# Optimization experiments

Hardware: AMD Instinct MI355X
Metric: run time of the kernel (lower is better)

The kernel has to match this reference:

```python
import jax, jax.numpy as jnp
import numpy as np
from jax import lax

B, N = 16, 4096
S1, S2, K = 512, 256, 32
EPS = 1e-5


def setup_inputs() -> dict:
    key = jax.random.key(0)
    ks = jax.random.split(key, 8)
    p = lambda k, shape: jax.random.normal(k, shape, jnp.float32) * 0.05
    return {
        "x": jax.random.normal(ks[0], (B, 3, N), jnp.float32),
        "w1": p(ks[1], (64, 3)),
        "w2": p(ks[2], (64, 64)),
        "g1": jnp.ones(64, jnp.float32), "b1": jnp.zeros(64, jnp.float32),
        "g2": jnp.ones(64, jnp.float32), "b2": jnp.zeros(64, jnp.float32),
        "sg1_w1": p(ks[3], (128, 128)), "sg1_w2": p(ks[4], (128, 128)),
        "sg1_g1": jnp.ones(128, jnp.float32), "sg1_b1": jnp.zeros(128, jnp.float32),
        "sg1_g2": jnp.ones(128, jnp.float32), "sg1_b2": jnp.zeros(128, jnp.float32),
        "sg2_w1": p(ks[5], (256, 256)), "sg2_w2": p(ks[6], (256, 256)),
        "sg2_g1": jnp.ones(256, jnp.float32), "sg2_b1": jnp.zeros(256, jnp.float32),
        "sg2_g2": jnp.ones(256, jnp.float32), "sg2_b2": jnp.zeros(256, jnp.float32),
    }


def fps(coords, s):
    # furthest point sampling, starts at index 0 (as pointnet2 CUDA kernel)
    Bc, Nc, _ = coords.shape
    def step(carry, _):
        dist, far = carry
        centroid = jnp.take_along_axis(coords, far[:, None, None], axis=1)  # [B,1,3]
        d = jnp.sum((coords - centroid) ** 2, -1)                            # [B,N]
        dist = jnp.minimum(dist, d)
        return (dist, jnp.argmax(dist, -1)), far
    init = (jnp.full((Bc, Nc), 1e10, coords.dtype), jnp.zeros((Bc,), jnp.int32))
    _, idxs = lax.scan(step, init, None, length=s)
    return idxs.T  # [B,s]


def gather(pts, idx):
    # pts [B,N,C], idx [B,...] -> [B,...,C]
    return jax.vmap(lambda p, i: p[i])(pts, idx)


def sqdist(a, b):
    # [B,S,3],[B,N,3] -> [B,S,N]
    return (jnp.sum(a ** 2, -1)[..., None] + jnp.sum(b ** 2, -1)[:, None, :]
            - 2.0 * jnp.einsum('bsc,bnc->bsn', a, b))


def bn_relu_grouped(y, g, b):
    # y [B,s,k,O]; BatchNorm1d over (B*s, O, k) => stats over (0,1,2)
    m = y.mean((0, 1, 2), keepdims=True)
    v = y.var((0, 1, 2), keepdims=True)
    return jax.nn.relu((y - m) / jnp.sqrt(v + EPS) * g + b)


def sg_block(f_bnc, coords, s, w1, g1, b1, w2, g2, b2):
    # f_bnc [B,N,C]; coords [B,N,3]
    fidx = fps(coords, s)                      # [B,s]
    new_xyz = gather(coords, fidx)             # [B,s,3]
    new_feat = gather(f_bnc, fidx)             # [B,s,C]
    d = sqdist(new_xyz, coords)                # [B,s,N]
    _, knn_idx = lax.top_k(-d, K)              # [B,s,K]
    grouped = gather(f_bnc, knn_idx)           # [B,s,K,C]
    center = new_feat[:, :, None]              # [B,s,1,C]
    agg = jnp.concatenate([grouped - center,
                           jnp.broadcast_to(center, grouped.shape)], -1)  # [B,s,K,2C]
    y = bn_relu_grouped(jnp.einsum('bskd,od->bsko', agg, w1), g1, b1)
    y = bn_relu_grouped(jnp.einsum('bskd,od->bsko', y, w2), g2, b2)
    return new_xyz, y.max(2)                   # [B,s,O]


def point_cbr(f, w, g, b):
    # f [B,C,N]; conv1d k=1 + BN (stats over (0,2)) + relu
    y = jnp.einsum('bcn,oc->bon', f, w)
    m = y.mean((0, 2), keepdims=True)
    v = y.var((0, 2), keepdims=True)
    return jax.nn.relu((y - m) / jnp.sqrt(v + EPS) * g[None, :, None] + b[None, :, None])


def reference(x, w1, w2, g1, b1, g2, b2,
              sg1_w1, sg1_w2, sg1_g1, sg1_b1, sg1_g2, sg1_b2,
              sg2_w1, sg2_w2, sg2_g1, sg2_b1, sg2_g2, sg2_b2):
    xyz = x.transpose(0, 2, 1)                                  # [B,N,3]
    f = point_cbr(point_cbr(x, w1, g1, b1), w2, g2, b2)         # [B,64,N]
    xyz1, f1 = sg_block(f.transpose(0, 2, 1), xyz, S1,
                        sg1_w1, sg1_g1, sg1_b1, sg1_w2, sg1_g2, sg1_b2)  # f1 [B,S1,128]
    _, f2 = sg_block(f1, xyz1, S2,
                     sg2_w1, sg2_g1, sg2_b1, sg2_w2, sg2_g2, sg2_b2)     # [B,S2,256]
    return f2.transpose(0, 2, 1)                                # [B,256,S2]
```

## Files before the change

### kernel.cpp

```cpp
#include <hip/hip_runtime.h>

#define EPSF 1e-5f
#define NBINS 64
#define STATS_REGION 32768

using short8  = __attribute__((ext_vector_type(8))) short;
using float4v = __attribute__((ext_vector_type(4))) float;

__device__ __forceinline__ unsigned short f2bf(float f){
    unsigned u = __float_as_uint(f);
    unsigned r = u + 0x7FFFu + ((u >> 16) & 1u);
    return (unsigned short)(r >> 16);
}
__device__ __forceinline__ float bf2f(unsigned short h){
    return __uint_as_float(((unsigned)h) << 16);
}
__device__ __forceinline__ unsigned monou(float f){
    unsigned u = __float_as_uint(f);
    return u ^ (((unsigned)((int)u >> 31)) | 0x80000000u);
}

template<int CTRL, int RMASK>
__device__ __forceinline__ float fmax_dpp(float x){
    int xi = __float_as_int(x);
    int yi = __builtin_amdgcn_update_dpp(xi, xi, CTRL, RMASK, 0xf, false);
    return fmaxf(x, __int_as_float(yi));
}
__device__ __forceinline__ float wave_max_dpp(float x){
    x = fmax_dpp<0x111, 0xf>(x);
    x = fmax_dpp<0x112, 0xf>(x);
    x = fmax_dpp<0x114, 0xf>(x);
    x = fmax_dpp<0x118, 0xf>(x);
    x = fmax_dpp<0x142, 0xa>(x);
    x = fmax_dpp<0x143, 0xc>(x);
    return __int_as_float(__builtin_amdgcn_readlane(__float_as_int(x), 63));
}


__global__ __launch_bounds__(256) void pc1_kernel(const float* __restrict__ x,
                                                  const float* __restrict__ w1,
                                                  float* __restrict__ y){
    __shared__ float w[192];
    int t = threadIdx.x;
    if (t < 192) w[t] = w1[t];
    __syncthreads();
    int gid = blockIdx.x * 256 + t;
    int b = gid >> 12;
    int n = gid & 4095;
    const float* xb = x + (size_t)b * 3 * 4096;
    float x0 = xb[n], x1 = xb[4096 + n], x2 = xb[8192 + n];
    float* yb = y + (size_t)b * 64 * 4096;
    #pragma unroll
    for (int o = 0; o < 64; o++){
        float v = x0 * w[o*3] + x1 * w[o*3+1] + x2 * w[o*3+2];
        yb[(size_t)o * 4096 + n] = v;
    }
}

template<int C, int NN>
__global__ __launch_bounds__(256) void stats_bcn_kernel(const float* __restrict__ y,
                                                        float* __restrict__ sums){
    int blk = blockIdx.x;
    int c = blk % C;
    const float* p = y + (size_t)blk * NN;
    float s = 0.f, q = 0.f;
    for (int i = threadIdx.x; i < NN; i += 256){ float v = p[i]; s += v; q += v*v; }
    for (int o = 32; o > 0; o >>= 1){ s += __shfl_down(s, o, 64); q += __shfl_down(q, o, 64); }
    __shared__ float ls[4], lq[4];
    int w = threadIdx.x >> 6;
    if ((threadIdx.x & 63) == 0){ ls[w] = s; lq[w] = q; }
    __syncthreads();
    if (threadIdx.x == 0){
        s = ls[0] + ls[1] + ls[2] + ls[3];
        q = lq[0] + lq[1] + lq[2] + lq[3];
        atomicAdd(&sums[c], s);
        atomicAdd(&sums[C + c], q);
    }
}

__global__ void bn_finalize_kernel(const float* __restrict__ sums,
                                   const float* __restrict__ g,
                                   const float* __restrict__ bb,
                                   float* __restrict__ ss, int C, int NB, float invCnt){
    int c = blockIdx.x * blockDim.x + threadIdx.x;
    if (c < C){
        float s = 0.f, q = 0.f;
        for (int bin = 0; bin < NB; bin++){
            s += sums[bin * 2 * C + c];
            q += sums[bin * 2 * C + C + c];
        }
        float m = s * invCnt;
        float v = q * invCnt - m * m;
        float sc = g[c] / sqrtf(v + EPSF);
        ss[c] = sc;
        ss[C + c] = bb[c] - m * sc;
    }
}

__global__ __launch_bounds__(256) void pc2_kernel(const float* __restrict__ y1,
                                                  const float* __restrict__ w2,
                                                  const float* __restrict__ ss,
                                                  float* __restrict__ y2){
    __shared__ float wt[64*64];
    __shared__ float lss[128];
    int t = threadIdx.x;
    for (int i = t; i < 4096; i += 256){ int o = i & 63, c = i >> 6; wt[c*64+o] = w2[o*64+c]; }
    if (t < 128) lss[t] = ss[t];
    __syncthreads();
    int gid = blockIdx.x * 256 + t;
    int b = gid >> 12, n = gid & 4095;
    const float* yb = y1 + (size_t)b * 64 * 4096;
    float acc[64];
    #pragma unroll
    for (int o = 0; o < 64; o++) acc[o] = 0.f;
    for (int c = 0; c < 64; c++){
        float v = yb[(size_t)c * 4096 + n];
        v = fmaxf(v * lss[c] + lss[64 + c], 0.f);
        #pragma unroll
        for (int o = 0; o < 64; o++) acc[o] += v * wt[c*64 + o];
    }
    float* ob = y2 + (size_t)b * 64 * 4096;
    #pragma unroll
    for (int o = 0; o < 64; o++) ob[(size_t)o * 4096 + n] = acc[o];
}

__global__ __launch_bounds__(256) void transpose_f_kernel(const float* __restrict__ y2,
                                                          const float* __restrict__ ss,
                                                          float* __restrict__ f){
    __shared__ float tile[64][65];
    __shared__ float lss[128];
    int t = threadIdx.x;
    if (t < 128) lss[t] = ss[t];
    __syncthreads();
    int blk = blockIdx.x;
    int b = blk >> 6;
    int nb = (blk & 63) * 64;
    const float* yb = y2 + (size_t)b * 64 * 4096;
    #pragma unroll
    for (int r = 0; r < 16; r++){
        int c = r * 4 + (t >> 6);
        int n = t & 63;
        float v = yb[(size_t)c * 4096 + nb + n];
        tile[c][n] = fmaxf(v * lss[c] + lss[64 + c], 0.f);
    }
    __syncthreads();
    float* fb = f + (size_t)b * 4096 * 64;
    #pragma unroll
    for (int r = 0; r < 16; r++){
        int n = r * 4 + (t >> 6);
        int c = t & 63;
        fb[(size_t)(nb + n) * 64 + c] = tile[c][n];
    }
}

template<int NP, int SO, int TPB, bool STRIDED>
__global__ __launch_bounds__(TPB) void fps_kernel(const float* __restrict__ coords,
                                                  int* __restrict__ fidx,
                                                  float* __restrict__ xyz_out){
    __shared__ float lx[NP], ly[NP], lz[NP];
    constexpr int W = TPB / 64;
    __shared__ unsigned long long red[2][W];
    const int b = blockIdx.x, t = threadIdx.x;
    constexpr int P = NP / TPB;
    const float* cb = coords + (size_t)b * 3 * NP;
    float px[P], py[P], pz[P], dist[P];
    #pragma unroll
    for (int i = 0; i < P; i++){
        int n = i * TPB + t;
        float X, Y, Z;
        if (STRIDED){ X = cb[n]; Y = cb[NP + n]; Z = cb[2*NP + n]; }
        else        { X = cb[n*3]; Y = cb[n*3+1]; Z = cb[n*3+2]; }
        lx[n] = X; ly[n] = Y; lz[n] = Z;
    }
    __syncthreads();
    #pragma unroll
    for (int i = 0; i < P; i++){
        int n = t * P + i;
        px[i] = lx[n]; py[i] = ly[n]; pz[i] = lz[n];
        dist[i] = 1e10f;
    }
    int cur = 0;
    for (int it = 0; it < SO; ++it){
        if (t == 0){
            fidx[b * SO + it] = cur;
            float* xo = xyz_out + ((size_t)b * SO + it) * 3;
            xo[0] = lx[cur]; xo[1] = ly[cur]; xo[2] = lz[cur];
        }
        float cx = lx[cur], cy = ly[cur], cz = lz[cur];
        float bd = -1.f;
        int bn = 0;
        {
            #pragma clang fp contract(off)
            #pragma unroll
            for (int i = 0; i < P; i++){
                float dx = px[i] - cx, dy = py[i] - cy, dz = pz[i] - cz;
                float d = (dx*dx + dy*dy) + dz*dz;
                float nd = fminf(dist[i], d);
                dist[i] = nd;
                if (nd > bd){ bd = nd; bn = t * P + i; }
            }
        }
        float wm = wave_max_dpp(bd);
        unsigned long long msk = __ballot(bd == wm);
        int wl = (int)(__ffsll(msk) - 1);
        int n_w = __builtin_amdgcn_readlane(bn, wl);
        if constexpr (W == 1){
            cur = n_w;
        } else {
            int par = it & 1;
            if ((t & 63) == 0){
                red[par][t >> 6] = ((unsigned long long)__float_as_uint(wm) << 32)
                                 | (unsigned)(0xFFFFFFFFu - (unsigned)n_w);
            }
            __syncthreads();
            unsigned long long best = red[par][0];
            #pragma unroll
            for (int j = 1; j < W; j++){
                unsigned long long v = red[par][j];
                best = best > v ? best : v;
            }
            cur = (int)(0xFFFFFFFFu - (unsigned)(best & 0xFFFFFFFFull));
        }
    }
}


template<int NC, int SO, bool STRIDED>
__global__ __launch_bounds__(64) void knn_kernel(const float* __restrict__ coords,
                                                 const float* __restrict__ samp,
                                                 int* __restrict__ knno){
    const int blk = blockIdx.x;
    const int b = blk / SO, s = blk % SO;
    const int lane = threadIdx.x;
    const float* cb = coords + (size_t)b * 3 * NC;
    const float* a = samp + ((size_t)b * SO + s) * 3;
    float ax = a[0], ay = a[1], az = a[2];
    float asq = ax*ax + ay*ay + az*az;
    constexpr int J = NC / 64;
    unsigned long long t8[8];
    #pragma unroll
    for (int i = 0; i < 8; i++) t8[i] = ~0ULL;
    for (int j = 0; j < J; j++){
        int n = j * 64 + lane;
        float bx, by, bz;
        if (STRIDED){ bx = cb[n]; by = cb[NC + n]; bz = cb[2*NC + n]; }
        else        { bx = cb[n*3]; by = cb[n*3+1]; bz = cb[n*3+2]; }
        float bsq = bx*bx + by*by + bz*bz;
        float dot = ax*bx + ay*by + az*bz;
        float d = (asq + bsq) - 2.0f * dot;
        unsigned long long key = ((unsigned long long)monou(d) << 32) | (unsigned)n;
        if (key < t8[7]){
            t8[7] = key;
            #pragma unroll
            for (int i = 6; i >= 0; i--){
                if (t8[i] > t8[i+1]){ unsigned long long tm = t8[i]; t8[i] = t8[i+1]; t8[i+1] = tm; }
            }
        }
    }
    unsigned long long cur = t8[0];
    int myout = 0;
    bool bad = false;
    int popped = 0;
    for (int r = 0; r < 32; r++){
        unsigned long long m = cur;
        #pragma unroll
        for (int o2 = 32; o2 > 0; o2 >>= 1){
            unsigned long long v = __shfl_xor(m, o2, 64);
            m = m < v ? m : v;
        }
        if (lane == r) myout = (int)(unsigned)(m & 0xFFFFFFFFull);
        if (cur == m){
            #pragma unroll
            for (int i = 0; i < 7; i++) t8[i] = t8[i+1];
            t8[7] = ~0ULL;
            cur = t8[0];
            popped++;
            if (J > 8 && popped == 8 && r < 31) bad = true;
        }
    }
    if (__any(bad)){
        unsigned long long last = 0;
        for (int r = 0; r < 32; r++){
            unsigned long long mk = ~0ULL;
            for (int j = 0; j < J; j++){
                int n = j * 64 + lane;
                float bx, by, bz;
                if (STRIDED){ bx = cb[n]; by = cb[NC + n]; bz = cb[2*NC + n]; }
                else        { bx = cb[n*3]; by = cb[n*3+1]; bz = cb[n*3+2]; }
                float bsq = bx*bx + by*by + bz*bz;
                float dot = ax*bx + ay*by + az*bz;
                float d = (asq + bsq) - 2.0f * dot;
                unsigned long long key = ((unsigned long long)monou(d) << 32) | (unsigned)n;
                if (key > last && key < mk) mk = key;
            }
            unsigned long long m = mk;
            #pragma unroll
            for (int o2 = 32; o2 > 0; o2 >>= 1){
                unsigned long long v = __shfl_xor(m, o2, 64);
                m = m < v ? m : v;
            }
            if (lane == r) myout = (int)(unsigned)(m & 0xFFFFFFFFull);
            last = m;
        }
    }
    if (lane < 32) knno[((size_t)b * SO + s) * 32 + lane] = myout;
}


template<int O, int D>
__global__ __launch_bounds__(256) void pack_w_kernel(const float* __restrict__ w,
                                                     unsigned short* __restrict__ pk){
    int tid = blockIdx.x * 256 + threadIdx.x;
    constexpr int CH = D / 32;
    constexpr int TOT = (O/16) * CH * 64;
    if (tid >= TOT) return;
    int lane = tid & 63;
    int fc = tid >> 6;
    int ch = fc % CH;
    int ot = fc / CH;
    int o  = ot * 16 + (lane & 15);
    int kb = ch * 32 + (lane >> 4) * 8;
    #pragma unroll
    for (int j = 0; j < 8; j++) pk[(size_t)tid * 8 + j] = f2bf(w[(size_t)o * D + kb + j]);
}

template<int D, int O>
__device__ __forceinline__ void mfma_compute_store(const short* A, const short* wp,
                                                   unsigned short* Y, float* lsum, float* lsq,
                                                   int blk, int t){
    constexpr int RS = D + 8;
    constexpr int CH = D / 32;
    constexpr int OT = O / 16;
    constexpr int OPW = OT / 4;
    int lane = t & 63, wv = t >> 6;
    int col = lane & 15, quad = lane >> 4;
    for (int oi = 0; oi < OPW; ++oi){
        int ot = wv * OPW + oi;
        for (int mt = 0; mt < 4; ++mt){
            float4v acc = {0.f, 0.f, 0.f, 0.f};
            #pragma unroll
            for (int ch = 0; ch < CH; ++ch){
                short8 a  = *(const short8*)(A + (mt*16 + col) * RS + ch*32 + quad*8);
                short8 bf = *(const short8*)(wp + ((size_t)(ot*CH + ch) * 64 + lane) * 8);
                acc = __builtin_amdgcn_mfma_f32_16x16x32_bf16(a, bf, acc, 0, 0, 0);
            }
            float s4 = 0.f, q4 = 0.f;
            size_t rowbase = (size_t)blk * 64 + mt * 16 + quad * 4;
            #pragma unroll
            for (int r = 0; r < 4; r++){
                float v = acc[r];
                s4 += v; q4 += v * v;
                Y[(rowbase + r) * O + ot * 16 + col] = f2bf(v);
            }
            s4 += __shfl_xor(s4, 16, 64); s4 += __shfl_xor(s4, 32, 64);
            q4 += __shfl_xor(q4, 16, 64); q4 += __shfl_xor(q4, 32, 64);
            if (quad == 0){ lsum[ot*16 + col] += s4; lsq[ot*16 + col] += q4; }
        }
    }
}

template<int DH, int O, int S, int NPTS>
__global__ __launch_bounds__(256) void gemm1_kernel(const float* __restrict__ fsrc,
                                                    const int* __restrict__ fidx,
                                                    const int* __restrict__ knn,
                                                    const short* __restrict__ wp,
                                                    unsigned short* __restrict__ Y,
                                                    float* __restrict__ sums){
    constexpr int D = 2 * DH;
    constexpr int RS = D + 8;
    __shared__ __align__(16) short A[64 * RS];
    __shared__ float lsum[O], lsq[O];
    int t = threadIdx.x;
    for (int i = t; i < O; i += 256){ lsum[i] = 0.f; lsq[i] = 0.f; }
    int blk = blockIdx.x;
    for (int g = 0; g < 2; ++g){
        int gid = blk * 2 + g;
        int b = gid / S;
        int cidx = fidx[gid];
        const float* fc = fsrc + ((size_t)b * NPTS + cidx) * DH;
        int kk = t >> 3;
        int p  = t & 7;
        int nb = knn[(size_t)gid * 32 + kk];
        const float* fn = fsrc + ((size_t)b * NPTS + nb) * DH;
        constexpr int E = D / 8;
        int d0 = p * E;
        short* row = A + (g * 32 + kk) * RS;
        #pragma unroll
        for (int e = 0; e < E; e++){
            int d = d0 + e;
            float v = (d < DH) ? (fn[d] - fc[d]) : fc[d - DH];
            row[d] = (short)f2bf(v);
        }
    }
    __syncthreads();
    mfma_compute_store<D, O>(A, wp, Y, lsum, lsq, blk, t);
    __syncthreads();
    float* dst = sums + (size_t)(blk & (NBINS - 1)) * 2 * O;
    for (int i = t; i < O; i += 256){
        atomicAdd(&dst[i], lsum[i]);
        atomicAdd(&dst[O + i], lsq[i]);
    }
}

template<int D, int O>
__global__ __launch_bounds__(256) void gemm2_kernel(const unsigned short* __restrict__ Yin,
                                                    const float* __restrict__ ss,
                                                    const short* __restrict__ wp,
                                                    unsigned short* __restrict__ Y,
                                                    float* __restrict__ sums){
    constexpr int RS = D + 8;
    __shared__ __align__(16) short A[64 * RS];
    __shared__ float lsum[O], lsq[O];
    __shared__ float lss[2 * D];
    int t = threadIdx.x;
    for (int i = t; i < O; i += 256){ lsum[i] = 0.f; lsq[i] = 0.f; }
    for (int i = t; i < 2*D; i += 256) lss[i] = ss[i];
    __syncthreads();
    int blk = blockIdx.x;
    {
        int row = t >> 2;
        int d0 = (t & 3) * (D / 4);
        const unsigned short* src = Yin + ((size_t)blk * 64 + row) * D + d0;
        short* dst = A + row * RS + d0;
        #pragma unroll
        for (int e = 0; e < D/4; e++){
            float v = bf2f(src[e]);
            int d = d0 + e;
            v = fmaxf(v * lss[d] + lss[D + d], 0.f);
            dst[e] = (short)f2bf(v);
        }
    }
    __syncthreads();
    mfma_compute_store<D, O>(A, wp, Y, lsum, lsq, blk, t);
    __syncthreads();
    float* dst = sums + (size_t)(blk & (NBINS - 1)) * 2 * O;
    for (int i = t; i < O; i += 256){
        atomicAdd(&dst[i], lsum[i]);
        atomicAdd(&dst[O + i], lsq[i]);
    }
}

template<int O>
__global__ __launch_bounds__(256) void maxk_kernel(const unsigned short* __restrict__ Y,
                                                   const float* __restrict__ ss,
                                                   float* __restrict__ out){
    int gid = blockIdx.x * 256 + threadIdx.x;
    int o = gid % O;
    int r = gid / O;
    float sc = ss[o], sh = ss[O + o];
    const unsigned short* p = Y + (size_t)r * 32 * O + o;
    float m = -1e30f;
    #pragma unroll 8
    for (int k = 0; k < 32; k++){
        float v = bf2f(p[(size_t)k * O]);
        m = fmaxf(m, v * sc + sh);
    }
    out[gid] = fmaxf(m, 0.f);
}

__global__ __launch_bounds__(256) void transpose_out_kernel(const float* __restrict__ in,
                                                            float* __restrict__ out){
    __shared__ float tile[64][65];
    int blk = blockIdx.x;
    int b = blk >> 4;
    int ot = (blk >> 2) & 3, st = blk & 3;
    int t = threadIdx.x;
    const float* ib = in + (size_t)b * 65536;
    float* ob = out + (size_t)b * 65536;
    #pragma unroll
    for (int r = 0; r < 16; r++){
        int srow = st * 64 + r * 4 + (t >> 6);
        int o = ot * 64 + (t & 63);
        tile[r * 4 + (t >> 6)][t & 63] = ib[srow * 256 + o];
    }
    __syncthreads();
    #pragma unroll
    for (int r = 0; r < 16; r++){
        int o = ot * 64 + r * 4 + (t >> 6);
        int srow = st * 64 + (t & 63);
        ob[o * 256 + srow] = tile[t & 63][r * 4 + (t >> 6)];
    }
}

extern "C" void kernel_launch(void* const* d_in, const int* in_sizes, int n_in,
                              void* d_out, int out_size, void* d_ws, size_t ws_size,
                              hipStream_t stream) {
    const float* x    = (const float*)d_in[0];
    const float* w1   = (const float*)d_in[1];
    const float* w2   = (const float*)d_in[2];
    const float* g1   = (const float*)d_in[3];
    const float* b1   = (const float*)d_in[4];
    const float* g2   = (const float*)d_in[5];
    const float* b2   = (const float*)d_in[6];
    const float* s1w1 = (const float*)d_in[7];
    const float* s1w2 = (const float*)d_in[8];
    const float* s1g1 = (const float*)d_in[9];
    const float* s1b1 = (const float*)d_in[10];
    const float* s1g2 = (const float*)d_in[11];
    const float* s1b2 = (const float*)d_in[12];
    const float* s2w1 = (const float*)d_in[13];
    const float* s2w2 = (const float*)d_in[14];
    const float* s2g1 = (const float*)d_in[15];
    const float* s2b1 = (const float*)d_in[16];
    const float* s2g2 = (const float*)d_in[17];
    const float* s2b2 = (const float*)d_in[18];
    float* out = (float*)d_out;

    char* ws = (char*)d_ws;
    size_t off = 0;
    auto take = [&](size_t bytes){ size_t r = off; off += (bytes + 255) & ~(size_t)255; return r; };
    float* f_buf   = (float*)(ws + take(16u*4096u*64u*4u));
    float* f1_buf  = (float*)(ws + take(16u*512u*128u*4u));
    int*   fidx1   = (int*)  (ws + take(16u*512u*4u));
    float* xyz1    = (float*)(ws + take(16u*512u*3u*4u));
    int*   fidx2   = (int*)  (ws + take(16u*256u*4u));
    float* xyz2    = (float*)(ws + take(16u*256u*3u*4u));
    int*   knn1    = (int*)  (ws + take(16u*512u*32u*4u));
    int*   knn2    = (int*)  (ws + take(16u*256u*32u*4u));
    unsigned short* wp1 = (unsigned short*)(ws + take(128u*128u*2u));
    unsigned short* wp2 = (unsigned short*)(ws + take(128u*128u*2u));
    unsigned short* wp3 = (unsigned short*)(ws + take(256u*256u*2u));
    unsigned short* wp4 = (unsigned short*)(ws + take(256u*256u*2u));
    float* stats   = (float*)(ws + take(6u*STATS_REGION*4u));
    float* ssb     = (float*)(ws + take(6u*1024u*4u));
    float* f2tmp   = (float*)(ws + take(16u*256u*256u*4u));
    char*  regA    = ws + take(67108864u);
    char*  regB    = ws + take(67108864u);
    (void)in_sizes; (void)n_in; (void)out_size; (void)ws_size;

    hipMemsetAsync(stats, 0, 6u*STATS_REGION*4u, stream);

    pack_w_kernel<128,128><<<8, 256, 0, stream>>>(s1w1, wp1);
    pack_w_kernel<128,128><<<8, 256, 0, stream>>>(s1w2, wp2);
    pack_w_kernel<256,256><<<32, 256, 0, stream>>>(s2w1, wp3);
    pack_w_kernel<256,256><<<32, 256, 0, stream>>>(s2w2, wp4);

    float* yA = (float*)regA;
    float* yB = (float*)regB;
    pc1_kernel<<<256, 256, 0, stream>>>(x, w1, yA);
    stats_bcn_kernel<64,4096><<<1024, 256, 0, stream>>>(yA, stats + 0*STATS_REGION);
    bn_finalize_kernel<<<1, 256, 0, stream>>>(stats + 0*STATS_REGION, g1, b1, ssb + 0*1024, 64, 1, 1.f/65536.f);
    pc2_kernel<<<256, 256, 0, stream>>>(yA, w2, ssb + 0*1024, yB);
    stats_bcn_kernel<64,4096><<<1024, 256, 0, stream>>>(yB, stats + 1*STATS_REGION);
    bn_finalize_kernel<<<1, 256, 0, stream>>>(stats + 1*STATS_REGION, g2, b2, ssb + 1*1024, 64, 1, 1.f/65536.f);
    transpose_f_kernel<<<1024, 256, 0, stream>>>(yB, ssb + 1*1024, f_buf);

    fps_kernel<4096,512,256,true><<<16, 256, 0, stream>>>(x, fidx1, xyz1);
    knn_kernel<4096,512,true><<<8192, 64, 0, stream>>>(x, xyz1, knn1);

    unsigned short* Y1 = (unsigned short*)regA;
    unsigned short* Y2 = (unsigned short*)regB;
    gemm1_kernel<64,128,512,4096><<<4096, 256, 0, stream>>>(f_buf, fidx1, knn1, (const short*)wp1, Y1, stats + 2*STATS_REGION);
    bn_finalize_kernel<<<1, 256, 0, stream>>>(stats + 2*STATS_REGION, s1g1, s1b1, ssb + 2*1024, 128, NBINS, 1.f/262144.f);
    gemm2_kernel<128,128><<<4096, 256, 0, stream>>>(Y1, ssb + 2*1024, (const short*)wp2, Y2, stats + 3*STATS_REGION);
    bn_finalize_kernel<<<1, 256, 0, stream>>>(stats + 3*STATS_REGION, s1g2, s1b2, ssb + 3*1024, 128, NBINS, 1.f/262144.f);
    maxk_kernel<128><<<4096, 256, 0, stream>>>(Y2, ssb + 3*1024, f1_buf);

    fps_kernel<512,256,64,false><<<16, 64, 0, stream>>>(xyz1, fidx2, xyz2);
    knn_kernel<512,256,false><<<4096, 64, 0, stream>>>(xyz1, xyz2, knn2);

    gemm1_kernel<128,256,256,512><<<2048, 256, 0, stream>>>(f1_buf, fidx2, knn2, (const short*)wp3, Y1, stats + 4*STATS_REGION);
    bn_finalize_kernel<<<1, 256, 0, stream>>>(stats + 4*STATS_REGION, s2g1, s2b1, ssb + 4*1024, 256, NBINS, 1.f/131072.f);
    gemm2_kernel<256,256><<<2048, 256, 0, stream>>>(Y1, ssb + 4*1024, (const short*)wp4, Y2, stats + 5*STATS_REGION);
    bn_finalize_kernel<<<1, 256, 0, stream>>>(stats + 5*STATS_REGION, s2g2, s2b2, ssb + 5*1024, 256, NBINS, 1.f/131072.f);
    maxk_kernel<256><<<4096, 256, 0, stream>>>(Y2, ssb + 5*1024, f2tmp);
    transpose_out_kernel<<<256, 256, 0, stream>>>(f2tmp, out);
}
```

Baseline: 1.080 ms.

## Fuse pointwise conv stages, compute BN1 stats analytically, fold BN finalize into consumers

Replaces the first two pointwise conv stages with a fused kernel. The first BatchNorm's mean and variance are derived analytically from the input's first and second moments, so the 64-channel intermediate is never materialized. The second conv output is written point-major, and its BN+ReLU is applied on the fly inside the grouping GEMM, removing the separate transpose pass. BN finalize kernels are folded into each consumer kernel, the final maxk+transpose are merged, and the four weight packers run as one launch. This cuts launches and global memory round trips, but every block now recomputes the BN scale over 64 bins, and the moment-based variance is numerically less robust.

```diff
diff --git a/kernel.cpp b/kernel.cpp
--- a/kernel.cpp
+++ b/kernel.cpp
@@ -36,120 +36,132 @@
     return __int_as_float(__builtin_amdgcn_readlane(__float_as_int(x), 63));
 }
 
-
-__global__ __launch_bounds__(256) void pc1_kernel(const float* __restrict__ x,
-                                                  const float* __restrict__ w1,
-                                                  float* __restrict__ y){
-    __shared__ float w[192];
-    int t = threadIdx.x;
-    if (t < 192) w[t] = w1[t];
-    __syncthreads();
-    int gid = blockIdx.x * 256 + t;
-    int b = gid >> 12;
-    int n = gid & 4095;
-    const float* xb = x + (size_t)b * 3 * 4096;
-    float x0 = xb[n], x1 = xb[4096 + n], x2 = xb[8192 + n];
-    float* yb = y + (size_t)b * 64 * 4096;
-    #pragma unroll
-    for (int o = 0; o < 64; o++){
-        float v = x0 * w[o*3] + x1 * w[o*3+1] + x2 * w[o*3+2];
-        yb[(size_t)o * 4096 + n] = v;
-    }
-}
-
-template<int C, int NN>
-__global__ __launch_bounds__(256) void stats_bcn_kernel(const float* __restrict__ y,
-                                                        float* __restrict__ sums){
-    int blk = blockIdx.x;
-    int c = blk % C;
-    const float* p = y + (size_t)blk * NN;
-    float s = 0.f, q = 0.f;
-    for (int i = threadIdx.x; i < NN; i += 256){ float v = p[i]; s += v; q += v*v; }
-    for (int o = 32; o > 0; o >>= 1){ s += __shfl_down(s, o, 64); q += __shfl_down(q, o, 64); }
-    __shared__ float ls[4], lq[4];
-    int w = threadIdx.x >> 6;
-    if ((threadIdx.x & 63) == 0){ ls[w] = s; lq[w] = q; }
-    __syncthreads();
-    if (threadIdx.x == 0){
-        s = ls[0] + ls[1] + ls[2] + ls[3];
-        q = lq[0] + lq[1] + lq[2] + lq[3];
-        atomicAdd(&sums[c], s);
-        atomicAdd(&sums[C + c], q);
-    }
-}
-
-__global__ void bn_finalize_kernel(const float* __restrict__ sums,
-                                   const float* __restrict__ g,
-                                   const float* __restrict__ bb,
-                                   float* __restrict__ ss, int C, int NB, float invCnt){
-    int c = blockIdx.x * blockDim.x + threadIdx.x;
-    if (c < C){
+__device__ __forceinline__ void compute_ss(const float* __restrict__ st,
+                                           const float* __restrict__ g,
+                                           const float* __restrict__ bb,
+                                           float* lss, int C, float invCnt,
+                                           int t, int TPB){
+    for (int c = t; c < C; c += TPB){
         float s = 0.f, q = 0.f;
-        for (int bin = 0; bin < NB; bin++){
-            s += sums[bin * 2 * C + c];
-            q += sums[bin * 2 * C + C + c];
+        for (int bin = 0; bin < NBINS; bin++){
+            s += st[bin * 2 * C + c];
+            q += st[bin * 2 * C + C + c];
         }
         float m = s * invCnt;
         float v = q * invCnt - m * m;
         float sc = g[c] / sqrtf(v + EPSF);
-        ss[c] = sc;
-        ss[C + c] = bb[c] - m * sc;
-    }
-}
-
-__global__ __launch_bounds__(256) void pc2_kernel(const float* __restrict__ y1,
-                                                  const float* __restrict__ w2,
-                                                  const float* __restrict__ ss,
-                                                  float* __restrict__ y2){
-    __shared__ float wt[64*64];
-    __shared__ float lss[128];
+        lss[c] = sc;
+        lss[C + c] = bb[c] - m * sc;
+    }
+}
+
+
+__global__ __launch_bounds__(1024) void stats_x_kernel(const float* __restrict__ x,
+                                                       float* __restrict__ xmom){
     int t = threadIdx.x;
+    float a[9] = {0,0,0,0,0,0,0,0,0};
+    for (int gid = t; gid < 65536; gid += 1024){
+        int b = gid >> 12, n = gid & 4095;
+        const float* xb = x + (size_t)b * 12288;
+        float x0 = xb[n], x1 = xb[4096 + n], x2 = xb[8192 + n];
+        a[0] += x0; a[1] += x1; a[2] += x2;
+        a[3] += x0*x0; a[4] += x0*x1; a[5] += x0*x2;
+        a[6] += x1*x1; a[7] += x1*x2; a[8] += x2*x2;
+    }
+    __shared__ float red[16][9];
+    #pragma unroll
+    for (int k = 0; k < 9; k++){
+        float v = a[k];
+        for (int o = 32; o > 0; o >>= 1) v += __shfl_down(v, o, 64);
+        a[k] = v;
+    }
+    if ((t & 63) == 0){
+        #pragma unroll
+        for (int k = 0; k < 9; k++) red[t >> 6][k] = a[k];
+    }
+    __syncthreads();
+    if (t == 0){
+        #pragma unroll
+        for (int k = 0; k < 9; k++){
+            float s = 0.f;
+            for (int w = 0; w < 16; w++) s += red[w][k];
+            xmom[k] = s;
+        }
+    }
+}
+
+__global__ __launch_bounds__(256) void pc_fused_kernel(const float* __restrict__ x,
+                                                       const float* __restrict__ w1,
+                                                       const float* __restrict__ w2,
+                                                       const float* __restrict__ g1,
+                                                       const float* __restrict__ b1,
+                                                       const float* __restrict__ xmom,
+                                                       float* __restrict__ y2t){
+    __shared__ float w1s[192];
+    __shared__ float wt[4096];
+    __shared__ float lss1[128];
+    int t = threadIdx.x;
+    if (t < 192) w1s[t] = w1[t];
     for (int i = t; i < 4096; i += 256){ int o = i & 63, c = i >> 6; wt[c*64+o] = w2[o*64+c]; }
-    if (t < 128) lss[t] = ss[t];
+    __syncthreads();
+    if (t < 64){
+        float mu0 = xmom[0] * (1.f/65536.f), mu1 = xmom[1] * (1.f/65536.f), mu2 = xmom[2] * (1.f/65536.f);
+        float M00 = xmom[3] * (1.f/65536.f), M01 = xmom[4] * (1.f/65536.f), M02 = xmom[5] * (1.f/65536.f);
+        float M11 = xmom[6] * (1.f/65536.f), M12 = xmom[7] * (1.f/65536.f), M22 = xmom[8] * (1.f/65536.f);
+        float a = w1s[t*3], b = w1s[t*3+1], c = w1s[t*3+2];
+        float mo = a*mu0 + b*mu1 + c*mu2;
+        float e2 = a*a*M00 + b*b*M11 + c*c*M22 + 2.f*(a*b*M01 + a*c*M02 + b*c*M12);
+        float var = e2 - mo*mo;
+        float sc = g1[t] / sqrtf(var + EPSF);
+        lss1[t] = sc;
+        lss1[64 + t] = b1[t] - mo * sc;
+    }
     __syncthreads();
     int gid = blockIdx.x * 256 + t;
     int b = gid >> 12, n = gid & 4095;
-    const float* yb = y1 + (size_t)b * 64 * 4096;
-    float acc[64];
-    #pragma unroll
-    for (int o = 0; o < 64; o++) acc[o] = 0.f;
+    const float* xb = x + (size_t)b * 12288;
+    float x0 = xb[n], x1 = xb[4096 + n], x2 = xb[8192 + n];
+    float h[64];
+    #pragma unroll
     for (int c = 0; c < 64; c++){
-        float v = yb[(size_t)c * 4096 + n];
-        v = fmaxf(v * lss[c] + lss[64 + c], 0.f);
+        float y1 = x0 * w1s[c*3] + x1 * w1s[c*3+1] + x2 * w1s[c*3+2];
+        h[c] = fmaxf(y1 * lss1[c] + lss1[64 + c], 0.f);
+    }
+    float4v acc[16];
+    #pragma unroll
+    for (int i = 0; i < 16; i++) acc[i] = (float4v){0.f,0.f,0.f,0.f};
+    for (int c = 0; c < 64; c++){
+        float hv = h[c];
         #pragma unroll
-        for (int o = 0; o < 64; o++) acc[o] += v * wt[c*64 + o];
-    }
-    float* ob = y2 + (size_t)b * 64 * 4096;
-    #pragma unroll
-    for (int o = 0; o < 64; o++) ob[(size_t)o * 4096 + n] = acc[o];
-}
-
-__global__ __launch_bounds__(256) void transpose_f_kernel(const float* __restrict__ y2,
-                                                          const float* __restrict__ ss,
-                                                          float* __restrict__ f){
-    __shared__ float tile[64][65];
-    __shared__ float lss[128];
-    int t = threadIdx.x;
-    if (t < 128) lss[t] = ss[t];
-    __syncthreads();
-    int blk = blockIdx.x;
-    int b = blk >> 6;
-    int nb = (blk & 63) * 64;
-    const float* yb = y2 + (size_t)b * 64 * 4096;
-    #pragma unroll
-    for (int r = 0; r < 16; r++){
-        int c = r * 4 + (t >> 6);
-        int n = t & 63;
-        float v = yb[(size_t)c * 4096 + nb + n];
-        tile[c][n] = fmaxf(v * lss[c] + lss[64 + c], 0.f);
-    }
-    __syncthreads();
-    float* fb = f + (size_t)b * 4096 * 64;
-    #pragma unroll
-    for (int r = 0; r < 16; r++){
-        int n = r * 4 + (t >> 6);
-        int c = t & 63;
-        fb[(size_t)(nb + n) * 64 + c] = tile[c][n];
+        for (int i = 0; i < 16; i++){
+            float4v w4 = *(const float4v*)&wt[c*64 + i*4];
+            acc[i] += hv * w4;
+        }
+    }
+    float* dst = y2t + (size_t)gid * 64;
+    #pragma unroll
+    for (int i = 0; i < 16; i++) *(float4v*)(dst + i*4) = acc[i];
+}
+
+__global__ __launch_bounds__(256) void stats_y2_kernel(const float* __restrict__ y2t,
+                                                       float* __restrict__ sums){
+    int t = threadIdx.x, blk = blockIdx.x;
+    int o = t & 63, rg = t >> 6;
+    float s = 0.f, q = 0.f;
+    for (int j = 0; j < 64; j++){
+        int row = blk * 256 + j * 4 + rg;
+        float v = y2t[(size_t)row * 64 + o];
+        s += v; q += v * v;
+    }
+    __shared__ float rs[4][64], rq[4][64];
+    rs[rg][o] = s; rq[rg][o] = q;
+    __syncthreads();
+    if (t < 64){
+        float ss = rs[0][t] + rs[1][t] + rs[2][t] + rs[3][t];
+        float qq = rq[0][t] + rq[1][t] + rq[2][t] + rq[3][t];
+        float* dst = sums + (size_t)(blk & (NBINS - 1)) * 128;
+        atomicAdd(&dst[t], ss);
+        atomicAdd(&dst[64 + t], qq);
     }
 }
 
@@ -308,9 +320,8 @@
 
 
 template<int O, int D>
-__global__ __launch_bounds__(256) void pack_w_kernel(const float* __restrict__ w,
-                                                     unsigned short* __restrict__ pk){
-    int tid = blockIdx.x * 256 + threadIdx.x;
+__device__ __forceinline__ void pack_body(const float* __restrict__ w,
+                                          unsigned short* __restrict__ pk, int tid){
     constexpr int CH = D / 32;
     constexpr int TOT = (O/16) * CH * 64;
     if (tid >= TOT) return;
@@ -322,6 +333,17 @@
     int kb = ch * 32 + (lane >> 4) * 8;
     #pragma unroll
     for (int j = 0; j < 8; j++) pk[(size_t)tid * 8 + j] = f2bf(w[(size_t)o * D + kb + j]);
+}
+
+__global__ __launch_bounds__(256) void pack_all_kernel(const float* w1, const float* w2,
+                                                       const float* w3, const float* w4,
+                                                       unsigned short* p1, unsigned short* p2,
+                                                       unsigned short* p3, unsigned short* p4){
+    int blk = blockIdx.x, t = threadIdx.x;
+    if (blk < 8)       pack_body<128,128>(w1, p1, blk * 256 + t);
+    else if (blk < 16) pack_body<128,128>(w2, p2, (blk - 8) * 256 + t);
+    else if (blk < 48) pack_body<256,256>(w3, p3, (blk - 16) * 256 + t);
+    else               pack_body<256,256>(w4, p4, (blk - 48) * 256 + t);
 }
 
 template<int D, int O>
@@ -359,8 +381,12 @@
     }
 }
 
-template<int DH, int O, int S, int NPTS>
+template<int DH, int O, int S, int NPTS, bool BN>
 __global__ __launch_bounds__(256) void gemm1_kernel(const float* __restrict__ fsrc,
+                                                    const float* __restrict__ fst,
+                                                    const float* __restrict__ fg,
+                                                    const float* __restrict__ fb,
+                                                    float finv,
                                                     const int* __restrict__ fidx,
                                                     const int* __restrict__ knn,
                                                     const short* __restrict__ wp,
@@ -370,8 +396,13 @@
     constexpr int RS = D + 8;
     __shared__ __align__(16) short A[64 * RS];
     __shared__ float lsum[O], lsq[O];
+    __shared__ float lssf[BN ? 2*DH : 1];
     int t = threadIdx.x;
     for (int i = t; i < O; i += 256){ lsum[i] = 0.f; lsq[i] = 0.f; }
+    if (BN){
+        compute_ss(fst, fg, fb, lssf, DH, finv, t, 256);
+        __syncthreads();
+    }
     int blk = blockIdx.x;
     for (int g = 0; g < 2; ++g){
         int gid = blk * 2 + g;
@@ -388,7 +419,19 @@
         #pragma unroll
         for (int e = 0; e < E; e++){
             int d = d0 + e;
-            float v = (d < DH) ? (fn[d] - fc[d]) : fc[d - DH];
+            float v;
+            if (d < DH){
+                float a = fn[d], c = fc[d];
+                if (BN){
+                    a = fmaxf(a * lssf[d] + lssf[DH + d], 0.f);
+                    c = fmaxf(c * lssf[d] + lssf[DH + d], 0.f);
+                }
+                v = a - c;
+            } else {
+                float c = fc[d - DH];
+                if (BN) c = fmaxf(c * lssf[d - DH] + lssf[DH + d - DH], 0.f);
+                v = c;
+            }
             row[d] = (short)f2bf(v);
         }
     }
@@ -404,7 +447,10 @@
 
 template<int D, int O>
 __global__ __launch_bounds__(256) void gemm2_kernel(const unsigned short* __restrict__ Yin,
-                                                    const float* __restrict__ ss,
+                                                    const float* __restrict__ st,
+                                                    const float* __restrict__ g,
+                                                    const float* __restrict__ bb,
+                                                    float inv,
                                                     const short* __restrict__ wp,
                                                     unsigned short* __restrict__ Y,
                                                     float* __restrict__ sums){
@@ -414,7 +460,7 @@
     __shared__ float lss[2 * D];
     int t = threadIdx.x;
     for (int i = t; i < O; i += 256){ lsum[i] = 0.f; lsq[i] = 0.f; }
-    for (int i = t; i < 2*D; i += 256) lss[i] = ss[i];
+    compute_ss(st, g, bb, lss, D, inv, t, 256);
     __syncthreads();
     int blk = blockIdx.x;
     {
@@ -442,12 +488,19 @@
 
 template<int O>
 __global__ __launch_bounds__(256) void maxk_kernel(const unsigned short* __restrict__ Y,
-                                                   const float* __restrict__ ss,
+                                                   const float* __restrict__ st,
+                                                   const float* __restrict__ g,
+                                                   const float* __restrict__ bb,
+                                                   float inv,
                                                    float* __restrict__ out){
-    int gid = blockIdx.x * 256 + threadIdx.x;
+    __shared__ float lss[2 * O];
+    int t = threadIdx.x;
+    compute_ss(st, g, bb, lss, O, inv, t, 256);
+    __syncthreads();
+    int gid = blockIdx.x * 256 + t;
     int o = gid % O;
     int r = gid / O;
-    float sc = ss[o], sh = ss[O + o];
+    float sc = lss[o], sh = lss[O + o];
     const unsigned short* p = Y + (size_t)r * 32 * O + o;
     float m = -1e30f;
     #pragma unroll 8
@@ -458,27 +511,40 @@
     out[gid] = fmaxf(m, 0.f);
 }
 
-__global__ __launch_bounds__(256) void transpose_out_kernel(const float* __restrict__ in,
-                                                            float* __restrict__ out){
+__global__ __launch_bounds__(256) void maxk_t_kernel(const unsigned short* __restrict__ Y,
+                                                     const float* __restrict__ st,
+                                                     const float* __restrict__ g,
+                                                     const float* __restrict__ bb,
+                                                     float inv,
+                                                     float* __restrict__ out){
+    __shared__ float lss[512];
     __shared__ float tile[64][65];
+    int t = threadIdx.x;
+    compute_ss(st, g, bb, lss, 256, inv, t, 256);
+    __syncthreads();
     int blk = blockIdx.x;
     int b = blk >> 4;
-    int ot = (blk >> 2) & 3, st = blk & 3;
-    int t = threadIdx.x;
-    const float* ib = in + (size_t)b * 65536;
-    float* ob = out + (size_t)b * 65536;
-    #pragma unroll
-    for (int r = 0; r < 16; r++){
-        int srow = st * 64 + r * 4 + (t >> 6);
-        int o = ot * 64 + (t & 63);
-        tile[r * 4 + (t >> 6)][t & 63] = ib[srow * 256 + o];
-    }
-    __syncthreads();
-    #pragma unroll
-    for (int r = 0; r < 16; r++){
-        int o = ot * 64 + r * 4 + (t >> 6);
-        int srow = st * 64 + (t & 63);
-        ob[o * 256 + srow] = tile[t & 63][r * 4 + (t >> 6)];
+    int ot = (blk >> 2) & 3, stt = blk & 3;
+    int o_in = t & 63, sg = t >> 6;
+    int o = ot * 64 + o_in;
+    float sc = lss[o], sh = lss[256 + o];
+    for (int si = 0; si < 16; si++){
+        int s = stt * 64 + sg * 16 + si;
+        int row = b * 256 + s;
+        const unsigned short* p = Y + ((size_t)row * 32) * 256 + o;
+        float m = -1e30f;
+        #pragma unroll 8
+        for (int k = 0; k < 32; k++){
+            float v = bf2f(p[(size_t)k * 256]);
+            m = fmaxf(m, v * sc + sh);
+        }
+        tile[sg * 16 + si][o_in] = fmaxf(m, 0.f);
+    }
+    __syncthreads();
+    int s_in = t & 63, og = t >> 6;
+    for (int oj = 0; oj < 16; oj++){
+        int oo = ot * 64 + og * 16 + oj;
+        out[(size_t)b * 65536 + (size_t)oo * 256 + stt * 64 + s_in] = tile[s_in][og * 16 + oj];
     }
 }
 
@@ -509,7 +575,7 @@
     char* ws = (char*)d_ws;
     size_t off = 0;
     auto take = [&](size_t bytes){ size_t r = off; off += (bytes + 255) & ~(size_t)255; return r; };
-    float* f_buf   = (float*)(ws + take(16u*4096u*64u*4u));
+    float* y2t     = (float*)(ws + take(16u*4096u*64u*4u));
     float* f1_buf  = (float*)(ws + take(16u*512u*128u*4u));
     int*   fidx1   = (int*)  (ws + take(16u*512u*4u));
     float* xyz1    = (float*)(ws + take(16u*512u*3u*4u));
@@ -522,47 +588,44 @@
     unsigned short* wp3 = (unsigned short*)(ws + take(256u*256u*2u));
     unsigned short* wp4 = (unsigned short*)(ws + take(256u*256u*2u));
     float* stats   = (float*)(ws + take(6u*STATS_REGION*4u));
-    float* ssb     = (float*)(ws + take(6u*1024u*4u));
-    float* f2tmp   = (float*)(ws + take(16u*256u*256u*4u));
     char*  regA    = ws + take(67108864u);
     char*  regB    = ws + take(67108864u);
     (void)in_sizes; (void)n_in; (void)out_size; (void)ws_size;
 
+    float* xmom    = stats + 0*STATS_REGION;
+    float* stY2    = stats + 1*STATS_REGION;
+    float* stG1a   = stats + 2*STATS_REGION;
+    float* stG2a   = stats + 3*STATS_REGION;
+    float* stG1b   = stats + 4*STATS_REGION;
+    float* stG2b   = stats + 5*STATS_REGION;
+
     hipMemsetAsync(stats, 0, 6u*STATS_REGION*4u, stream);
 
-    pack_w_kernel<128,128><<<8, 256, 0, stream>>>(s1w1, wp1);
-    pack_w_kernel<128,128><<<8, 256, 0, stream>>>(s1w2, wp2);
-    pack_w_kernel<256,256><<<32, 256, 0, stream>>>(s2w1, wp3);
-    pack_w_kernel<256,256><<<32, 256, 0, stream>>>(s2w2, wp4);
-
-    float* yA = (float*)regA;
-    float* yB = (float*)regB;
-    pc1_kernel<<<256, 256, 0, stream>>>(x, w1, yA);
-    stats_bcn_kernel<64,4096><<<1024, 256, 0, stream>>>(yA, stats + 0*STATS_REGION);
-    bn_finalize_kernel<<<1, 256, 0, stream>>>(stats + 0*STATS_REGION, g1, b1, ssb + 0*1024, 64, 1, 1.f/65536.f);
-    pc2_kernel<<<256, 256, 0, stream>>>(yA, w2, ssb + 0*1024, yB);
-    stats_bcn_kernel<64,4096><<<1024, 256, 0, stream>>>(yB, stats + 1*STATS_REGION);
-    bn_finalize_kernel<<<1, 256, 0, stream>>>(stats + 1*STATS_REGION, g2, b2, ssb + 1*1024, 64, 1, 1.f/65536.f);
-    transpose_f_kernel<<<1024, 256, 0, stream>>>(yB, ssb + 1*1024, f_buf);
+    pack_all_kernel<<<80, 256, 0, stream>>>(s1w1, s1w2, s2w1, s2w2, wp1, wp2, wp3, wp4);
+
+    stats_x_kernel<<<1, 1024, 0, stream>>>(x, xmom);
+    pc_fused_kernel<<<256, 256, 0, stream>>>(x, w1, w2, g1, b1, xmom, y2t);
+    stats_y2_kernel<<<256, 256, 0, stream>>>(y2t, stY2);
 
     fps_kernel<4096,512,256,true><<<16, 256, 0, stream>>>(x, fidx1, xyz1);
     knn_kernel<4096,512,true><<<8192, 64, 0, stream>>>(x, xyz1, knn1);
 
     unsigned short* Y1 = (unsigned short*)regA;
     unsigned short* Y2 = (unsigned short*)regB;
-    gemm1_kernel<64,128,512,4096><<<4096, 256, 0, stream>>>(f_buf, fidx1, knn1, (const short*)wp1, Y1, stats + 2*STATS_REGION);
-    bn_finalize_kernel<<<1, 256, 0, stream>>>(stats + 2*STATS_REGION, s1g1, s1b1, ssb + 2*1024, 128, NBINS, 1.f/262144.f);
-    gemm2_kernel<128,128><<<4096, 256, 0, stream>>>(Y1, ssb + 2*1024, (const short*)wp2, Y2, stats + 3*STATS_REGION);
-    bn_finalize_kernel<<<1, 256, 0, stream>>>(stats + 3*STATS_REGION, s1g2, s1b2, ssb + 3*1024, 128, NBINS, 1.f/262144.f);
-    maxk_kernel<128><<<4096, 256, 0, stream>>>(Y2, ssb + 3*1024, f1_buf);
+    gemm1_kernel<64,128,512,4096,true><<<4096, 256, 0, stream>>>(
+        y2t, stY2, g2, b2, 1.f/65536.f, fidx1, knn1, (const short*)wp1, Y1, stG1a);
+    gemm2_kernel<128,128><<<4096, 256, 0, stream>>>(
+        Y1, stG1a, s1g1, s1b1, 1.f/262144.f, (const short*)wp2, Y2, stG2a);
+    maxk_kernel<128><<<4096, 256, 0, stream>>>(
+        Y2, stG2a, s1g2, s1b2, 1.f/262144.f, f1_buf);
 
     fps_kernel<512,256,64,false><<<16, 64, 0, stream>>>(xyz1, fidx2, xyz2);
     knn_kernel<512,256,false><<<4096, 64, 0, stream>>>(xyz1, xyz2, knn2);
 
-    gemm1_kernel<128,256,256,512><<<2048, 256, 0, stream>>>(f1_buf, fidx2, knn2, (const short*)wp3, Y1, stats + 4*STATS_REGION);
-    bn_finalize_kernel<<<1, 256, 0, stream>>>(stats + 4*STATS_REGION, s2g1, s2b1, ssb + 4*1024, 256, NBINS, 1.f/131072.f);
-    gemm2_kernel<256,256><<<2048, 256, 0, stream>>>(Y1, ssb + 4*1024, (const short*)wp4, Y2, stats + 5*STATS_REGION);
-    bn_finalize_kernel<<<1, 256, 0, stream>>>(stats + 5*STATS_REGION, s2g2, s2b2, ssb + 5*1024, 256, NBINS, 1.f/131072.f);
-    maxk_kernel<256><<<4096, 256, 0, stream>>>(Y2, ssb + 5*1024, f2tmp);
-    transpose_out_kernel<<<256, 256, 0, stream>>>(f2tmp, out);
-}
+    gemm1_kernel<128,256,256,512,false><<<2048, 256, 0, stream>>>(
+        f1_buf, nullptr, nullptr, nullptr, 0.f, fidx2, knn2, (const short*)wp3, Y1, stG1b);
+    gemm2_kernel<256,256><<<2048, 256, 0, stream>>>(
+        Y1, stG1b, s2g1, s2b1, 1.f/131072.f, (const short*)wp4, Y2, stG2b);
+    maxk_t_kernel<<<256, 256, 0, stream>>>(
+        Y2, stG2b, s2g2, s2b2, 1.f/131072.f, out);
+}
```

Result: slower. 1.105 ms (+2.3%).
